# Kernel tuning notes

Measured on AMD Instinct MI355X. Metric: run time of the kernel, lower is better.

## Reference

```python
import jax, jax.numpy as jnp
from jax import lax
import numpy as np

IN, HID, OUT = 28, 64, 10


def _lstm_layer(x_seq, W_ih, W_hh, b_ih, b_hh):
    # x_seq: [B, T, in]; PyTorch gate order: i, f, g, o (stacked along 4H)
    B = x_seq.shape[0]
    H = W_hh.shape[1]
    # Precompute input projection for all timesteps: [B, T, 4H]
    x_proj = jnp.einsum('bti,gi->btg', x_seq, W_ih) + b_ih + b_hh

    def step(carry, xt):
        h, c = carry
        gates = xt + h @ W_hh.T  # [B, 4H]
        i, f, g, o = jnp.split(gates, 4, axis=-1)
        i = jax.nn.sigmoid(i)
        f = jax.nn.sigmoid(f)
        g = jnp.tanh(g)
        o = jax.nn.sigmoid(o)
        c = f * c + i * g
        h = o * jnp.tanh(c)
        return (h, c), h

    h0 = jnp.zeros((B, H), x_seq.dtype)
    (_, _), hs = lax.scan(step, (h0, h0), jnp.swapaxes(x_proj, 0, 1))
    return jnp.swapaxes(hs, 0, 1)  # [B, T, H]


def setup_inputs() -> dict:
    key = jax.random.key(0)
    ks = jax.random.split(key, 12)
    s_in = 1.0 / np.sqrt(HID)
    u = lambda k, shape: jax.random.uniform(k, shape, jnp.float32, -s_in, s_in)
    return {
        'x': jax.random.normal(ks[0], (16384, 1, 28, 28), jnp.float32),
        'W_ih0': u(ks[1], (4 * HID, IN)),
        'W_hh0': u(ks[2], (4 * HID, HID)),
        'b_ih0': u(ks[3], (4 * HID,)),
        'b_hh0': u(ks[4], (4 * HID,)),
        'W_ih1': u(ks[5], (4 * HID, HID)),
        'W_hh1': u(ks[6], (4 * HID, HID)),
        'b_ih1': u(ks[7], (4 * HID,)),
        'b_hh1': u(ks[8], (4 * HID,)),
        'W_lin': u(ks[9], (OUT, HID)),
        'b_lin': u(ks[10], (OUT,)),
    }


def reference(x, W_ih0, W_hh0, b_ih0, b_hh0, W_ih1, W_hh1, b_ih1, b_hh1, W_lin, b_lin):
    # (N, C, H, W) -> (N, C*H, W): sequence of rows, feature = W = 28
    x = x.reshape(x.shape[0], -1, x.shape[-1])
    h1 = _lstm_layer(x, W_ih0, W_hh0, b_ih0, b_hh0)   # [B, T, 64]
    h2 = _lstm_layer(h1, W_ih1, W_hh1, b_ih1, b_hh1)  # [B, T, 64]
    last = h2[:, -1, :]
    return last @ W_lin.T + b_lin  # [B, 10]
```

## Files before the change

kernel.cpp:

```cpp
#include <hip/hip_runtime.h>


typedef _Float16 half8 __attribute__((ext_vector_type(8)));
typedef float floatx4 __attribute__((ext_vector_type(4)));

#define NFRAG 112
#define WS_BIAS_OFF (NFRAG * 1024)
#define K2 2.8853900817779268f

#if __has_builtin(__builtin_amdgcn_exp2f)
#define EXP2(v) __builtin_amdgcn_exp2f(v)
#else
#define EXP2(v) __expf(0.6931471805599453f * (v))
#endif
#define RCP(v) __builtin_amdgcn_rcpf(v)

__global__ void prep_kernel(const float* __restrict__ Wih0, const float* __restrict__ Whh0,
                            const float* __restrict__ bih0, const float* __restrict__ bhh0,
                            const float* __restrict__ Wih1, const float* __restrict__ Whh1,
                            const float* __restrict__ bih1, const float* __restrict__ bhh1,
                            _Float16* __restrict__ wA, float* __restrict__ wBias) {
    int idx = blockIdx.x * blockDim.x + threadIdx.x;
    if (idx < NFRAG * 512) {
        int f = idx >> 9, slot = idx & 511;
        int lane = slot >> 3, j = slot & 7;
        int mt, kt, layer;
        if (f < 48) { layer = 0; mt = f / 3; kt = f % 3; }
        else        { layer = 1; int f2 = f - 48; mt = f2 >> 2; kt = f2 & 3; }
        int m = mt * 16 + (lane & 15);
        int k = kt * 32 + (lane >> 4) * 8 + j;
        int u = m >> 2, g = m & 3;
        int row = g * 64 + u;
        float v;
        if (layer == 0) {
            if (k < 28)       v = Wih0[row * 28 + k];
            else if (k == 28) v = bih0[row] + bhh0[row];
            else if (k < 32)  v = 0.f;
            else              v = Whh0[row * 64 + (k - 32)];
        } else {
            if (k < 64)       v = Wih1[row * 64 + k];
            else              v = Whh1[row * 64 + (k - 64)];
        }
        float s = (g == 2) ? K2 : -1.4426950408889634f;
        wA[idx] = (_Float16)(v * s);
    } else if (idx < NFRAG * 512 + 256) {
        int m = idx - NFRAG * 512;
        int g = m & 3;
        int row = g * 64 + (m >> 2);
        float s = (g == 2) ? K2 : -1.4426950408889634f;
        wBias[m] = (bih1[row] + bhh1[row]) * s;
    }
}

template <int N>
__device__ __forceinline__ void gate_batch(const floatx4* acc, float* c,
                                           _Float16* const* planes, const int* offs) {
    float ei[N], ef[N], eg[N], eo[N];
    #pragma unroll
    for (int i = 0; i < N; ++i) {
        floatx4 a = acc[i];
        ei[i] = EXP2(a[0]);
        ef[i] = EXP2(a[1]);
        eg[i] = EXP2(a[2]);
        eo[i] = EXP2(a[3]);
    }
    float ri[N], rf[N], rg[N], ro[N];
    #pragma unroll
    for (int i = 0; i < N; ++i) {
        ri[i] = RCP(1.0f + ei[i]);
        rf[i] = RCP(1.0f + ef[i]);
        rg[i] = RCP(1.0f + eg[i]);
        ro[i] = RCP(1.0f + eo[i]);
    }
    float ec[N];
    #pragma unroll
    for (int i = 0; i < N; ++i) {
        float tg = 1.0f - 2.0f * rg[i];
        float cn = rf[i] * c[i] + ri[i] * tg;
        c[i] = cn;
        ec[i] = EXP2(K2 * cn);
    }
    #pragma unroll
    for (int i = 0; i < N; ++i) {
        float tc = 1.0f - 2.0f * RCP(ec[i] + 1.0f);
        planes[i][offs[i]] = (_Float16)(ro[i] * tc);
    }
}

__launch_bounds__(1024, 4)
__global__ void lstm_mfma(const float* __restrict__ x,
                          const _Float16* __restrict__ wA,
                          const float* __restrict__ wBias,
                          const float* __restrict__ Wlin, const float* __restrict__ blin,
                          float* __restrict__ out) {
    __shared__ __align__(16) _Float16 h0p[2][2][2048];
    __shared__ __align__(16) _Float16 h1p[2][2][2048];
    __shared__ __align__(16) _Float16 xb[2][2][1024];
    __shared__ float wlin_s[640];
    __shared__ float blin_s[10];

    const int lane = threadIdx.x;
    const int w    = threadIdx.y;
    const int tid  = w * 64 + lane;
    const int quad = lane >> 4;
    const int col  = lane & 15;
    const int u    = 4 * w + quad;

    half8 A0[3], A1[4];
    #pragma unroll
    for (int kt = 0; kt < 3; ++kt)
        A0[kt] = *(const half8*)(wA + (w * 3 + kt) * 512 + lane * 8);
    #pragma unroll
    for (int kt = 0; kt < 4; ++kt)
        A1[kt] = *(const half8*)(wA + (48 + w * 4 + kt) * 512 + lane * 8);
    const floatx4 bias1 = *(const floatx4*)(wBias + u * 4);

    int xrd[2], hrd[2][2], hwr[2];
    #pragma unroll
    for (int in = 0; in < 2; ++in) {
        xrd[in] = in * 512 + lane * 8;
        #pragma unroll
        for (int kt = 0; kt < 2; ++kt) hrd[kt][in] = (in * 2 + kt) * 512 + lane * 8;
        hwr[in] = (in * 2 + (u >> 5)) * 512 + (((u >> 3) & 3) * 16 + col) * 8 + (u & 7);
    }

    const int xi = tid & 31;
    const bool xvalid = xi < 28;
    const int xbi = tid >> 5;
    const float* xg = x + (blockIdx.x * 64 + xbi) * 784 + xi;
    const int xstg = (xbi >> 4) * 512 + ((xi >> 3) * 16 + (xbi & 15)) * 8 + (xi & 7);

    {
        ((int*)&h0p[0][1][0])[tid] = 0;
        ((int*)&h0p[1][1][0])[tid] = 0;
        ((int*)&h1p[0][1][0])[tid] = 0;
        ((int*)&h1p[1][1][0])[tid] = 0;
        float xv0 = xvalid ? xg[0] : 0.f;
        float xv1 = xvalid ? xg[32 * 784] : 0.f;
        xb[0][0][xstg] = (xi == 28) ? (_Float16)1.0f : (_Float16)xv0;
        xb[1][0][xstg] = (xi == 28) ? (_Float16)1.0f : (_Float16)xv1;
    }
    __syncthreads();

    float c0[2][2] = {{0.f, 0.f}, {0.f, 0.f}};
    float c1[2][2] = {{0.f, 0.f}, {0.f, 0.f}};

    for (int p = -1; p <= 27; ++p) {
        const int pr  = p & 1;
        const int pr1 = pr ^ 1;
        const bool doL0 = (p < 27);
        const bool doL1 = (p >= 0);

        float xn[2] = {0.f, 0.f};
        if (p <= 25 && xvalid) {
            xn[0] = xg[(p + 2) * 28];
            xn[1] = xg[32 * 784 + (p + 2) * 28];
        }

        half8 bx[2][2], bh0[2][2][2];
        if (doL0) {
            #pragma unroll
            for (int G = 0; G < 2; ++G)
                #pragma unroll
                for (int in = 0; in < 2; ++in)
                    bx[G][in] = *(const half8*)&xb[G][pr1][xrd[in]];
        }
        #pragma unroll
        for (int G = 0; G < 2; ++G)
            #pragma unroll
            for (int kt = 0; kt < 2; ++kt)
                #pragma unroll
                for (int in = 0; in < 2; ++in)
                    bh0[G][kt][in] = *(const half8*)&h0p[G][pr][hrd[kt][in]];

        floatx4 acc0[2][2], acc1[2][2];
        if (doL0) {
            #pragma unroll
            for (int G = 0; G < 2; ++G)
                #pragma unroll
                for (int in = 0; in < 2; ++in) {
                    acc0[G][in] = __builtin_amdgcn_mfma_f32_16x16x32_f16(
                                      A0[0], bx[G][in], (floatx4){0.f, 0.f, 0.f, 0.f}, 0, 0, 0);
                    #pragma unroll
                    for (int kt = 0; kt < 2; ++kt)
                        acc0[G][in] = __builtin_amdgcn_mfma_f32_16x16x32_f16(
                                          A0[kt + 1], bh0[G][kt][in], acc0[G][in], 0, 0, 0);
                }
        }
        if (doL1) {
            #pragma unroll
            for (int G = 0; G < 2; ++G)
                #pragma unroll
                for (int in = 0; in < 2; ++in) {
                    acc1[G][in] = bias1;
                    #pragma unroll
                    for (int kt = 0; kt < 2; ++kt)
                        acc1[G][in] = __builtin_amdgcn_mfma_f32_16x16x32_f16(
                                          A1[kt], bh0[G][kt][in], acc1[G][in], 0, 0, 0);
                }

            half8 bh1[2][2][2];
            #pragma unroll
            for (int G = 0; G < 2; ++G)
                #pragma unroll
                for (int kt = 0; kt < 2; ++kt)
                    #pragma unroll
                    for (int in = 0; in < 2; ++in)
                        bh1[G][kt][in] = *(const half8*)&h1p[G][pr1][hrd[kt][in]];
            #pragma unroll
            for (int G = 0; G < 2; ++G)
                #pragma unroll
                for (int kt = 0; kt < 2; ++kt)
                    #pragma unroll
                    for (int in = 0; in < 2; ++in)
                        acc1[G][in] = __builtin_amdgcn_mfma_f32_16x16x32_f16(
                                          A1[kt + 2], bh1[G][kt][in], acc1[G][in], 0, 0, 0);
        }

        if (doL0 && doL1) {
            floatx4 a8[8] = {acc0[0][0], acc0[0][1], acc1[0][0], acc1[0][1],
                             acc0[1][0], acc0[1][1], acc1[1][0], acc1[1][1]};
            float   cc[8] = {c0[0][0], c0[0][1], c1[0][0], c1[0][1],
                             c0[1][0], c0[1][1], c1[1][0], c1[1][1]};
            _Float16* pl[8] = {h0p[0][pr1], h0p[0][pr1], h1p[0][pr], h1p[0][pr],
                               h0p[1][pr1], h0p[1][pr1], h1p[1][pr], h1p[1][pr]};
            int offs[8] = {hwr[0], hwr[1], hwr[0], hwr[1],
                           hwr[0], hwr[1], hwr[0], hwr[1]};
            gate_batch<8>(a8, cc, pl, offs);
            c0[0][0] = cc[0]; c0[0][1] = cc[1]; c1[0][0] = cc[2]; c1[0][1] = cc[3];
            c0[1][0] = cc[4]; c0[1][1] = cc[5]; c1[1][0] = cc[6]; c1[1][1] = cc[7];
        } else if (doL0) {
            floatx4 a4[4] = {acc0[0][0], acc0[0][1], acc0[1][0], acc0[1][1]};
            float   cc[4] = {c0[0][0], c0[0][1], c0[1][0], c0[1][1]};
            _Float16* pl[4] = {h0p[0][pr1], h0p[0][pr1], h0p[1][pr1], h0p[1][pr1]};
            int offs[4] = {hwr[0], hwr[1], hwr[0], hwr[1]};
            gate_batch<4>(a4, cc, pl, offs);
            c0[0][0] = cc[0]; c0[0][1] = cc[1]; c0[1][0] = cc[2]; c0[1][1] = cc[3];
        } else {
            floatx4 a4[4] = {acc1[0][0], acc1[0][1], acc1[1][0], acc1[1][1]};
            float   cc[4] = {c1[0][0], c1[0][1], c1[1][0], c1[1][1]};
            _Float16* pl[4] = {h1p[0][pr], h1p[0][pr], h1p[1][pr], h1p[1][pr]};
            int offs[4] = {hwr[0], hwr[1], hwr[0], hwr[1]};
            gate_batch<4>(a4, cc, pl, offs);
            c1[0][0] = cc[0]; c1[0][1] = cc[1]; c1[1][0] = cc[2]; c1[1][1] = cc[3];
        }

        if (p <= 25) {
            xb[0][pr][xstg] = (xi == 28) ? (_Float16)1.0f : (_Float16)xn[0];
            xb[1][pr][xstg] = (xi == 28) ? (_Float16)1.0f : (_Float16)xn[1];
        }
        __syncthreads();
    }

    if (tid < 640) wlin_s[tid] = Wlin[tid];
    if (tid < 10)  blin_s[tid] = blin[tid];
    __syncthreads();
    if (tid < 640) {
        int b = tid / 10, o = tid - b * 10;
        int G = b >> 5, bl = b & 31;
        float a = blin_s[o];
        #pragma unroll 8
        for (int uu = 0; uu < 64; ++uu) {
            float hv = (float)h1p[G][1][((bl >> 4) * 2 + (uu >> 5)) * 512 + (((uu >> 3) & 3) * 16 + (bl & 15)) * 8 + (uu & 7)];
            a += wlin_s[o * 64 + uu] * hv;
        }
        out[(blockIdx.x * 64 + b) * 10 + o] = a;
    }
}

extern "C" void kernel_launch(void* const* d_in, const int* in_sizes, int n_in,
                              void* d_out, int out_size, void* d_ws, size_t ws_size,
                              hipStream_t stream) {
    const float* x    = (const float*)d_in[0];
    const float* Wih0 = (const float*)d_in[1];
    const float* Whh0 = (const float*)d_in[2];
    const float* bih0 = (const float*)d_in[3];
    const float* bhh0 = (const float*)d_in[4];
    const float* Wih1 = (const float*)d_in[5];
    const float* Whh1 = (const float*)d_in[6];
    const float* bih1 = (const float*)d_in[7];
    const float* bhh1 = (const float*)d_in[8];
    const float* Wlin = (const float*)d_in[9];
    const float* blin = (const float*)d_in[10];
    float* out = (float*)d_out;

    _Float16* wA    = (_Float16*)d_ws;
    float*    wBias = (float*)((char*)d_ws + WS_BIAS_OFF);

    prep_kernel<<<225, 256, 0, stream>>>(Wih0, Whh0, bih0, bhh0,
                                         Wih1, Whh1, bih1, bhh1, wA, wBias);
    lstm_mfma<<<256, dim3(64, 16), 0, stream>>>(x, wA, wBias, Wlin, blin, out);
}
```

Before: 178.4 us.

## Halve block batch to 32 with 8 waves each owning two M-tiles; fuse gate reciprocals

Each block now processes 32 sequences with 8 waves instead of 64 with 16. Each wave holds weight fragments for two M-tiles and reuses one set of B fragments across them, which doubles the grid to 512 blocks and cuts LDS per block. The gate math is rewritten algebraically so one reciprocal yields the new cell state and another yields h, using fewer RCP instructions. The risks are more register pressure from the doubled A fragments and reduced range safety in the combined products (overflow of exp products for large pre-activations).

```diff
diff --git a/kernel.cpp b/kernel.cpp
--- a/kernel.cpp
+++ b/kernel.cpp
@@ -64,38 +64,41 @@
         eg[i] = EXP2(a[2]);
         eo[i] = EXP2(a[3]);
     }
-    float ri[N], rf[N], rg[N], ro[N];
-    #pragma unroll
-    for (int i = 0; i < N; ++i) {
-        ri[i] = RCP(1.0f + ei[i]);
-        rf[i] = RCP(1.0f + ef[i]);
-        rg[i] = RCP(1.0f + eg[i]);
-        ro[i] = RCP(1.0f + eo[i]);
+    float num[N], rd[N], po[N];
+    #pragma unroll
+    for (int i = 0; i < N; ++i) {
+        float pi = 1.0f + ei[i];
+        float pf = 1.0f + ef[i];
+        float pg = 1.0f + eg[i];
+        po[i] = 1.0f + eo[i];
+        float m = pg * pi;
+        num[i] = c[i] * m + (eg[i] - 1.0f) * pf;
+        rd[i]  = RCP(pf * m);
     }
     float ec[N];
     #pragma unroll
     for (int i = 0; i < N; ++i) {
-        float tg = 1.0f - 2.0f * rg[i];
-        float cn = rf[i] * c[i] + ri[i] * tg;
+        float cn = num[i] * rd[i];
         c[i] = cn;
         ec[i] = EXP2(K2 * cn);
     }
     #pragma unroll
     for (int i = 0; i < N; ++i) {
-        float tc = 1.0f - 2.0f * RCP(ec[i] + 1.0f);
-        planes[i][offs[i]] = (_Float16)(ro[i] * tc);
-    }
-}
-
-__launch_bounds__(1024, 4)
+        float r2 = RCP(ec[i] * po[i] + po[i]);
+        float h = (ec[i] - 1.0f) * r2;
+        planes[i][offs[i]] = (_Float16)h;
+    }
+}
+
+__launch_bounds__(512, 4)
 __global__ void lstm_mfma(const float* __restrict__ x,
                           const _Float16* __restrict__ wA,
                           const float* __restrict__ wBias,
                           const float* __restrict__ Wlin, const float* __restrict__ blin,
                           float* __restrict__ out) {
-    __shared__ __align__(16) _Float16 h0p[2][2][2048];
-    __shared__ __align__(16) _Float16 h1p[2][2][2048];
-    __shared__ __align__(16) _Float16 xb[2][2][1024];
+    __shared__ __align__(16) _Float16 h0p[2][2048];
+    __shared__ __align__(16) _Float16 h1p[2][2048];
+    __shared__ __align__(16) _Float16 xb[2][1024];
     __shared__ float wlin_s[640];
     __shared__ float blin_s[10];
 
@@ -104,41 +107,49 @@
     const int tid  = w * 64 + lane;
     const int quad = lane >> 4;
     const int col  = lane & 15;
-    const int u    = 4 * w + quad;
-
-    half8 A0[3], A1[4];
-    #pragma unroll
-    for (int kt = 0; kt < 3; ++kt)
-        A0[kt] = *(const half8*)(wA + (w * 3 + kt) * 512 + lane * 8);
-    #pragma unroll
-    for (int kt = 0; kt < 4; ++kt)
-        A1[kt] = *(const half8*)(wA + (48 + w * 4 + kt) * 512 + lane * 8);
-    const floatx4 bias1 = *(const floatx4*)(wBias + u * 4);
-
-    int xrd[2], hrd[2][2], hwr[2];
+
+    half8 A0[2][3], A1[2][4];
+    floatx4 bias1[2];
+    int hwr[2][2];
+    #pragma unroll
+    for (int j = 0; j < 2; ++j) {
+        const int MT = 2 * w + j;
+        #pragma unroll
+        for (int kt = 0; kt < 3; ++kt)
+            A0[j][kt] = *(const half8*)(wA + (MT * 3 + kt) * 512 + lane * 8);
+        #pragma unroll
+        for (int kt = 0; kt < 4; ++kt)
+            A1[j][kt] = *(const half8*)(wA + (48 + MT * 4 + kt) * 512 + lane * 8);
+        const int u = MT * 4 + quad;
+        bias1[j] = *(const floatx4*)(wBias + u * 4);
+        #pragma unroll
+        for (int in = 0; in < 2; ++in)
+            hwr[j][in] = (in * 2 + (u >> 5)) * 512 + (((u >> 3) & 3) * 16 + col) * 8 + (u & 7);
+    }
+
+    int xrd[2], hrd[2][2];
     #pragma unroll
     for (int in = 0; in < 2; ++in) {
         xrd[in] = in * 512 + lane * 8;
         #pragma unroll
         for (int kt = 0; kt < 2; ++kt) hrd[kt][in] = (in * 2 + kt) * 512 + lane * 8;
-        hwr[in] = (in * 2 + (u >> 5)) * 512 + (((u >> 3) & 3) * 16 + col) * 8 + (u & 7);
     }
 
     const int xi = tid & 31;
     const bool xvalid = xi < 28;
     const int xbi = tid >> 5;
-    const float* xg = x + (blockIdx.x * 64 + xbi) * 784 + xi;
-    const int xstg = (xbi >> 4) * 512 + ((xi >> 3) * 16 + (xbi & 15)) * 8 + (xi & 7);
+    const float* xg = x + (blockIdx.x * 32 + xbi) * 784 + xi;
+    const int xstg = ((xi >> 3) * 16 + xbi) * 8 + (xi & 7);
 
     {
-        ((int*)&h0p[0][1][0])[tid] = 0;
-        ((int*)&h0p[1][1][0])[tid] = 0;
-        ((int*)&h1p[0][1][0])[tid] = 0;
-        ((int*)&h1p[1][1][0])[tid] = 0;
+        ((int*)&h0p[1][0])[tid * 2 + 0] = 0;
+        ((int*)&h0p[1][0])[tid * 2 + 1] = 0;
+        ((int*)&h1p[1][0])[tid * 2 + 0] = 0;
+        ((int*)&h1p[1][0])[tid * 2 + 1] = 0;
         float xv0 = xvalid ? xg[0] : 0.f;
-        float xv1 = xvalid ? xg[32 * 784] : 0.f;
-        xb[0][0][xstg] = (xi == 28) ? (_Float16)1.0f : (_Float16)xv0;
-        xb[1][0][xstg] = (xi == 28) ? (_Float16)1.0f : (_Float16)xv1;
+        float xv1 = xvalid ? xg[16 * 784] : 0.f;
+        xb[0][xstg]       = (xi == 28) ? (_Float16)1.0f : (_Float16)xv0;
+        xb[0][xstg + 512] = (xi == 28) ? (_Float16)1.0f : (_Float16)xv1;
     }
     __syncthreads();
 
@@ -151,120 +162,114 @@
         const bool doL0 = (p < 27);
         const bool doL1 = (p >= 0);
 
-        float xn[2] = {0.f, 0.f};
+        float xn0 = 0.f, xn1 = 0.f;
         if (p <= 25 && xvalid) {
-            xn[0] = xg[(p + 2) * 28];
-            xn[1] = xg[32 * 784 + (p + 2) * 28];
-        }
-
-        half8 bx[2][2], bh0[2][2][2];
+            xn0 = xg[(p + 2) * 28];
+            xn1 = xg[16 * 784 + (p + 2) * 28];
+        }
+
+        half8 bx[2], bh0[2][2];
         if (doL0) {
             #pragma unroll
-            for (int G = 0; G < 2; ++G)
-                #pragma unroll
-                for (int in = 0; in < 2; ++in)
-                    bx[G][in] = *(const half8*)&xb[G][pr1][xrd[in]];
-        }
-        #pragma unroll
-        for (int G = 0; G < 2; ++G)
-            #pragma unroll
-            for (int kt = 0; kt < 2; ++kt)
-                #pragma unroll
-                for (int in = 0; in < 2; ++in)
-                    bh0[G][kt][in] = *(const half8*)&h0p[G][pr][hrd[kt][in]];
+            for (int in = 0; in < 2; ++in)
+                bx[in] = *(const half8*)&xb[pr1][xrd[in]];
+        }
+        #pragma unroll
+        for (int kt = 0; kt < 2; ++kt)
+            #pragma unroll
+            for (int in = 0; in < 2; ++in)
+                bh0[kt][in] = *(const half8*)&h0p[pr][hrd[kt][in]];
 
         floatx4 acc0[2][2], acc1[2][2];
         if (doL0) {
             #pragma unroll
-            for (int G = 0; G < 2; ++G)
+            for (int j = 0; j < 2; ++j)
                 #pragma unroll
                 for (int in = 0; in < 2; ++in) {
-                    acc0[G][in] = __builtin_amdgcn_mfma_f32_16x16x32_f16(
-                                      A0[0], bx[G][in], (floatx4){0.f, 0.f, 0.f, 0.f}, 0, 0, 0);
+                    acc0[j][in] = __builtin_amdgcn_mfma_f32_16x16x32_f16(
+                                      A0[j][0], bx[in], (floatx4){0.f, 0.f, 0.f, 0.f}, 0, 0, 0);
                     #pragma unroll
                     for (int kt = 0; kt < 2; ++kt)
-                        acc0[G][in] = __builtin_amdgcn_mfma_f32_16x16x32_f16(
-                                          A0[kt + 1], bh0[G][kt][in], acc0[G][in], 0, 0, 0);
+                        acc0[j][in] = __builtin_amdgcn_mfma_f32_16x16x32_f16(
+                                          A0[j][kt + 1], bh0[kt][in], acc0[j][in], 0, 0, 0);
                 }
         }
         if (doL1) {
             #pragma unroll
-            for (int G = 0; G < 2; ++G)
+            for (int j = 0; j < 2; ++j)
                 #pragma unroll
                 for (int in = 0; in < 2; ++in) {
-                    acc1[G][in] = bias1;
+                    acc1[j][in] = bias1[j];
                     #pragma unroll
                     for (int kt = 0; kt < 2; ++kt)
-                        acc1[G][in] = __builtin_amdgcn_mfma_f32_16x16x32_f16(
-                                          A1[kt], bh0[G][kt][in], acc1[G][in], 0, 0, 0);
+                        acc1[j][in] = __builtin_amdgcn_mfma_f32_16x16x32_f16(
+                                          A1[j][kt], bh0[kt][in], acc1[j][in], 0, 0, 0);
                 }
 
-            half8 bh1[2][2][2];
-            #pragma unroll
-            for (int G = 0; G < 2; ++G)
+            half8 bh1[2][2];
+            #pragma unroll
+            for (int kt = 0; kt < 2; ++kt)
+                #pragma unroll
+                for (int in = 0; in < 2; ++in)
+                    bh1[kt][in] = *(const half8*)&h1p[pr1][hrd[kt][in]];
+            #pragma unroll
+            for (int j = 0; j < 2; ++j)
                 #pragma unroll
                 for (int kt = 0; kt < 2; ++kt)
                     #pragma unroll
                     for (int in = 0; in < 2; ++in)
-                        bh1[G][kt][in] = *(const half8*)&h1p[G][pr1][hrd[kt][in]];
-            #pragma unroll
-            for (int G = 0; G < 2; ++G)
-                #pragma unroll
-                for (int kt = 0; kt < 2; ++kt)
-                    #pragma unroll
-                    for (int in = 0; in < 2; ++in)
-                        acc1[G][in] = __builtin_amdgcn_mfma_f32_16x16x32_f16(
-                                          A1[kt + 2], bh1[G][kt][in], acc1[G][in], 0, 0, 0);
+                        acc1[j][in] = __builtin_amdgcn_mfma_f32_16x16x32_f16(
+                                          A1[j][kt + 2], bh1[kt][in], acc1[j][in], 0, 0, 0);
         }
 
         if (doL0 && doL1) {
-            floatx4 a8[8] = {acc0[0][0], acc0[0][1], acc1[0][0], acc1[0][1],
-                             acc0[1][0], acc0[1][1], acc1[1][0], acc1[1][1]};
-            float   cc[8] = {c0[0][0], c0[0][1], c1[0][0], c1[0][1],
-                             c0[1][0], c0[1][1], c1[1][0], c1[1][1]};
-            _Float16* pl[8] = {h0p[0][pr1], h0p[0][pr1], h1p[0][pr], h1p[0][pr],
-                               h0p[1][pr1], h0p[1][pr1], h1p[1][pr], h1p[1][pr]};
-            int offs[8] = {hwr[0], hwr[1], hwr[0], hwr[1],
-                           hwr[0], hwr[1], hwr[0], hwr[1]};
+            floatx4 a8[8] = {acc0[0][0], acc0[0][1], acc0[1][0], acc0[1][1],
+                             acc1[0][0], acc1[0][1], acc1[1][0], acc1[1][1]};
+            float   cc[8] = {c0[0][0], c0[0][1], c0[1][0], c0[1][1],
+                             c1[0][0], c1[0][1], c1[1][0], c1[1][1]};
+            _Float16* pl[8] = {h0p[pr1], h0p[pr1], h0p[pr1], h0p[pr1],
+                               h1p[pr],  h1p[pr],  h1p[pr],  h1p[pr]};
+            int offs[8] = {hwr[0][0], hwr[0][1], hwr[1][0], hwr[1][1],
+                           hwr[0][0], hwr[0][1], hwr[1][0], hwr[1][1]};
             gate_batch<8>(a8, cc, pl, offs);
-            c0[0][0] = cc[0]; c0[0][1] = cc[1]; c1[0][0] = cc[2]; c1[0][1] = cc[3];
-            c0[1][0] = cc[4]; c0[1][1] = cc[5]; c1[1][0] = cc[6]; c1[1][1] = cc[7];
+            c0[0][0] = cc[0]; c0[0][1] = cc[1]; c0[1][0] = cc[2]; c0[1][1] = cc[3];
+            c1[0][0] = cc[4]; c1[0][1] = cc[5]; c1[1][0] = cc[6]; c1[1][1] = cc[7];
         } else if (doL0) {
             floatx4 a4[4] = {acc0[0][0], acc0[0][1], acc0[1][0], acc0[1][1]};
             float   cc[4] = {c0[0][0], c0[0][1], c0[1][0], c0[1][1]};
-            _Float16* pl[4] = {h0p[0][pr1], h0p[0][pr1], h0p[1][pr1], h0p[1][pr1]};
-            int offs[4] = {hwr[0], hwr[1], hwr[0], hwr[1]};
+            _Float16* pl[4] = {h0p[pr1], h0p[pr1], h0p[pr1], h0p[pr1]};
+            int offs[4] = {hwr[0][0], hwr[0][1], hwr[1][0], hwr[1][1]};
             gate_batch<4>(a4, cc, pl, offs);
             c0[0][0] = cc[0]; c0[0][1] = cc[1]; c0[1][0] = cc[2]; c0[1][1] = cc[3];
         } else {
             floatx4 a4[4] = {acc1[0][0], acc1[0][1], acc1[1][0], acc1[1][1]};
             float   cc[4] = {c1[0][0], c1[0][1], c1[1][0], c1[1][1]};
-            _Float16* pl[4] = {h1p[0][pr], h1p[0][pr], h1p[1][pr], h1p[1][pr]};
-            int offs[4] = {hwr[0], hwr[1], hwr[0], hwr[1]};
+            _Float16* pl[4] = {h1p[pr], h1p[pr], h1p[pr], h1p[pr]};
+            int offs[4] = {hwr[0][0], hwr[0][1], hwr[1][0], hwr[1][1]};
             gate_batch<4>(a4, cc, pl, offs);
             c1[0][0] = cc[0]; c1[0][1] = cc[1]; c1[1][0] = cc[2]; c1[1][1] = cc[3];
         }
 
         if (p <= 25) {
-            xb[0][pr][xstg] = (xi == 28) ? (_Float16)1.0f : (_Float16)xn[0];
-            xb[1][pr][xstg] = (xi == 28) ? (_Float16)1.0f : (_Float16)xn[1];
+            xb[pr][xstg]       = (xi == 28) ? (_Float16)1.0f : (_Float16)xn0;
+            xb[pr][xstg + 512] = (xi == 28) ? (_Float16)1.0f : (_Float16)xn1;
         }
         __syncthreads();
     }
 
-    if (tid < 640) wlin_s[tid] = Wlin[tid];
+    wlin_s[tid] = Wlin[tid];
+    if (tid < 128) wlin_s[512 + tid] = Wlin[512 + tid];
     if (tid < 10)  blin_s[tid] = blin[tid];
     __syncthreads();
-    if (tid < 640) {
+    if (tid < 320) {
         int b = tid / 10, o = tid - b * 10;
-        int G = b >> 5, bl = b & 31;
         float a = blin_s[o];
         #pragma unroll 8
         for (int uu = 0; uu < 64; ++uu) {
-            float hv = (float)h1p[G][1][((bl >> 4) * 2 + (uu >> 5)) * 512 + (((uu >> 3) & 3) * 16 + (bl & 15)) * 8 + (uu & 7)];
+            float hv = (float)h1p[1][((b >> 4) * 2 + (uu >> 5)) * 512 + (((uu >> 3) & 3) * 16 + (b & 15)) * 8 + (uu & 7)];
             a += wlin_s[o * 64 + uu] * hv;
         }
-        out[(blockIdx.x * 64 + b) * 10 + o] = a;
+        out[(blockIdx.x * 32 + b) * 10 + o] = a;
     }
 }
 
@@ -289,5 +294,5 @@
 
     prep_kernel<<<225, 256, 0, stream>>>(Wih0, Whh0, bih0, bhh0,
                                          Wih1, Whh1, bih1, bhh1, wA, wBias);
-    lstm_mfma<<<256, dim3(64, 16), 0, stream>>>(x, wA, wBias, Wlin, blin, out);
-}
+    lstm_mfma<<<512, dim3(64, 8), 0, stream>>>(x, wA, wBias, Wlin, blin, out);
+}
```

Measured after the change: 171.6 us. 1.04x faster.
